# Optimization experiments

Hardware: AMD Instinct MI355X
Metric: run time of the kernel (lower is better)

Reference implementation:

```python
import jax, jax.numpy as jnp
import numpy as np

N = 100000          # nodes (src == target here)
E = 1600000         # edges, avg degree 16
C_IN = 128
C_OUT = 128
R = 7               # num_edge_types
T = 4               # num_node_types


def setup_inputs() -> dict:
    key = jax.random.key(0)
    ks = jax.random.split(key, 7)
    x = jax.random.normal(ks[0], (N, C_IN), dtype=jnp.float32)
    edge_index = jax.random.randint(ks[1], (2, E), 0, N, dtype=jnp.int32)
    edge_type = jax.random.randint(ks[2], (E,), 0, R, dtype=jnp.int32)
    target_node_type = jax.random.randint(ks[3], (N,), 0, T, dtype=jnp.int32)
    # Linear weights: rel_lins (no bias), root_lins (with bias); torch Linear: y = x @ W.T + b
    rel_w = jax.random.normal(ks[4], (R, C_OUT, C_IN), dtype=jnp.float32) * (1.0 / np.sqrt(C_IN))
    root_w = jax.random.normal(ks[5], (T, C_OUT, C_IN), dtype=jnp.float32) * (1.0 / np.sqrt(C_IN))
    root_b = jax.random.normal(ks[6], (T, C_OUT), dtype=jnp.float32) * 0.01
    return {"x": x, "edge_index": edge_index, "edge_type": edge_type,
            "target_node_type": target_node_type,
            "rel_w": rel_w, "root_w": root_w, "root_b": root_b}


def reference(x, edge_index, edge_type, target_node_type, rel_w, root_w, root_b):
    # Per-edge-type gather -> (bias-free) linear -> scatter-mean.
    # linear commutes with mean (no bias), so aggregate first, then apply W_r.
    n = x.shape[0]
    src, dst = edge_index[0], edge_index[1]
    x_j = x[src]                                   # [E, C_in] gather
    seg = dst.astype(jnp.int32) * R + edge_type    # fused (node, edge_type) segment id
    sums = jax.ops.segment_sum(x_j, seg, num_segments=n * R).reshape(n, R, C_IN)
    cnt = jax.ops.segment_sum(jnp.ones((x_j.shape[0],), x.dtype), seg,
                              num_segments=n * R).reshape(n, R)
    means = sums / jnp.maximum(cnt, 1.0)[:, :, None]   # zero rows stay zero (PyG mean of empty = 0)
    out = jnp.einsum('nrc,roc->no', means, rel_w)       # sum_r rel_lins[r](mean_r)
    # Per-node-type root linear with bias (small loop over T=4 types).
    for t in range(T):
        m = (target_node_type == t).astype(x.dtype)[:, None]
        out = out + m * (x @ root_w[t].T + root_b[t])
    return out
```

## Files before the change

kernel.cpp:

```cpp
#include <hip/hip_runtime.h>

#define N_NODES 100000
#define N_EDGES 1600000
#define C_DIM   128
#define R_TYPES 7
#define T_TYPES 4
#define SEGS    (N_NODES * R_TYPES)
#define NB_E    (N_EDGES / 256)
#define NB_N    ((N_NODES + 255) / 256)
#define XP_ROWS 100096
#define DST_PART 12500
#define NB_ROOT ((N_NODES + 63) / 64)

#define OFF_CNTI   0ull
#define OFF_INV    2800000ull
#define OFF_DOFF   5600000ull
#define OFF_CURS   6000004ull
#define OFF_MISC   6400004ull
#define OFF_PERM   6400132ull
#define PERM_CAP   100288
#define OFF_BLKN   6801284ull
#define OFF_BSUM   6813796ull
#define OFF_ESRC   6815360ull
#define OFF_XP     13215360ull
#define OFF_WF     38839936ull
#define OFF_XWB    39069312ull
#define XWB_PLANE  ((size_t)XP_ROWS * 128)
#define FULL_NEED  218441344ull
#define FB_NEED    64693888ull
#define OFF_WRF    OFF_PERM

typedef __attribute__((ext_vector_type(8))) short short8;
typedef __attribute__((ext_vector_type(4))) float f32x4;

__device__ inline unsigned short f2bf(float f) {
    unsigned int u = __float_as_uint(f);
    u += 0x7fffu + ((u >> 16) & 1u);
    return (unsigned short)(u >> 16);
}
__device__ inline float bf2f(unsigned int h) { return __uint_as_float(h << 16); }

__global__ void edge_hist(const int* __restrict__ ei, const int* __restrict__ et,
                          int* __restrict__ cnti) {
    int e = blockIdx.x * 256 + threadIdx.x;
    atomicAdd(&cnti[ei[N_EDGES + e] * R_TYPES + et[e]], 1);
}

__global__ void inv_kernel(const int* __restrict__ cnti, float* __restrict__ inv) {
    int i = blockIdx.x * blockDim.x + threadIdx.x;
    if (i < SEGS) inv[i] = 1.0f / (float)max(cnti[i], 1);
}

__global__ void dst_scan1(const int* __restrict__ cnti, int* __restrict__ dst_off,
                          int* __restrict__ bsum) {
    __shared__ int sbuf[256];
    int tid = threadIdx.x;
    int i = blockIdx.x * 256 + tid;
    int v = 0;
    if (i < N_NODES) {
        #pragma unroll
        for (int r = 0; r < R_TYPES; ++r) v += cnti[i * R_TYPES + r];
    }
    sbuf[tid] = v;
    __syncthreads();
    #pragma unroll
    for (int off = 1; off < 256; off <<= 1) {
        int t = (tid >= off) ? sbuf[tid - off] : 0;
        __syncthreads();
        sbuf[tid] += t;
        __syncthreads();
    }
    int incl = sbuf[tid];
    if (i < N_NODES) dst_off[i] = incl - v;
    if (tid == 255) bsum[blockIdx.x] = incl;
}

__global__ void seg_scan2(int* __restrict__ bsum, int nb) {
    __shared__ int sbuf[256];
    int tid = threadIdx.x;
    int running = 0;
    for (int c0 = 0; c0 < nb; c0 += 256) {
        int b = c0 + tid;
        int v = (b < nb) ? bsum[b] : 0;
        sbuf[tid] = v;
        __syncthreads();
        #pragma unroll
        for (int off = 1; off < 256; off <<= 1) {
            int t = (tid >= off) ? sbuf[tid - off] : 0;
            __syncthreads();
            sbuf[tid] += t;
            __syncthreads();
        }
        int incl = sbuf[tid];
        int tot = sbuf[255];
        __syncthreads();
        if (b < nb) bsum[b] = running + incl - v;
        running += tot;
    }
}

__global__ void dst_scan3(int* __restrict__ dst_off, int* __restrict__ cursor,
                          const int* __restrict__ bsum) {
    int i = blockIdx.x * 256 + threadIdx.x;
    if (i < N_NODES) {
        int val = dst_off[i] + bsum[blockIdx.x];
        dst_off[i] = val;
        cursor[i] = val;
    }
    if (i == 0) dst_off[N_NODES] = N_EDGES;
}

__global__ void place_edges(const int* __restrict__ ei, const int* __restrict__ et,
                            int* __restrict__ cursor, int* __restrict__ esrc) {
    int p = blockIdx.x & 7;
    int e = (blockIdx.x >> 3) * 256 + threadIdx.x;
    int d = ei[N_EDGES + e];
    if (d / DST_PART != p) return;
    int pos = atomicAdd(&cursor[d], 1);
    int r = et[e];
    esrc[pos] = (r << 20) | (r * XP_ROWS + ei[e]);
}

__global__ void cvt_x_frag(const float* __restrict__ x, unsigned short* __restrict__ xp) {
    int id = blockIdx.x * 256 + threadIdx.x;
    int n = id >> 4, ko = id & 15;
    short8 o;
    if (n < N_NODES) {
        const float4* px = (const float4*)(x + (size_t)n * C_DIM + ko * 8);
        float4 a = px[0], b = px[1];
        o[0] = (short)f2bf(a.x); o[1] = (short)f2bf(a.y);
        o[2] = (short)f2bf(a.z); o[3] = (short)f2bf(a.w);
        o[4] = (short)f2bf(b.x); o[5] = (short)f2bf(b.y);
        o[6] = (short)f2bf(b.z); o[7] = (short)f2bf(b.w);
    } else {
        o = (short8)0;
    }
    size_t off = (size_t)(n >> 4) * 2048 + (ko >> 2) * 512 + (ko & 3) * 128 + (n & 15) * 8;
    *(short8*)(xp + off) = o;
}

__global__ void cvt_w_frag(const float* __restrict__ rel_w, unsigned short* __restrict__ wf) {
    int id = blockIdx.x * 256 + threadIdx.x;
    if (id >= R_TYPES * 128 * 16) return;
    int r = id >> 11, rest = id & 2047;
    int o = rest >> 4, ko = rest & 15;
    const float4* pw = (const float4*)(rel_w + (size_t)r * 16384 + o * 128 + ko * 8);
    float4 a = pw[0], b = pw[1];
    short8 v;
    v[0] = (short)f2bf(a.x); v[1] = (short)f2bf(a.y);
    v[2] = (short)f2bf(a.z); v[3] = (short)f2bf(a.w);
    v[4] = (short)f2bf(b.x); v[5] = (short)f2bf(b.y);
    v[6] = (short)f2bf(b.z); v[7] = (short)f2bf(b.w);
    size_t off = (size_t)r * 16384 + (o >> 4) * 2048 + (ko >> 2) * 512 + (ko & 3) * 128 + (o & 15) * 8;
    *(short8*)(wf + off) = v;
}

__global__ void cvt_rootw_frag(const float* __restrict__ root_w, unsigned short* __restrict__ wrf) {
    int id = blockIdx.x * 256 + threadIdx.x;
    if (id >= T_TYPES * 128 * 16) return;
    int t = id >> 11, rest = id & 2047;
    int o = rest >> 4, ko = rest & 15;
    const float4* pw = (const float4*)(root_w + (size_t)t * 16384 + o * 128 + ko * 8);
    float4 a = pw[0], b = pw[1];
    float v[8] = {a.x, a.y, a.z, a.w, b.x, b.y, b.z, b.w};
    short8 hi, lo;
    #pragma unroll
    for (int j = 0; j < 8; ++j) {
        unsigned short h = f2bf(v[j]);
        hi[j] = (short)h;
        lo[j] = (short)f2bf(v[j] - bf2f(h));
    }
    size_t off = (size_t)t * 16384 + (o >> 4) * 2048 + (ko >> 2) * 512 + (ko & 3) * 128 + (o & 15) * 8;
    *(short8*)(wrf + off) = hi;
    *(short8*)(wrf + (size_t)T_TYPES * 16384 + off) = lo;
}

__launch_bounds__(256)
__global__ void root_nat(const float* __restrict__ x, const unsigned short* __restrict__ wrf,
                         const float* __restrict__ root_b, const int* __restrict__ tnt,
                         float* __restrict__ out) {
    __shared__ int cnt[T_TYPES];
    __shared__ int goff[T_TYPES];
    __shared__ int rankb[64];
    __shared__ int lidx[112];
    __shared__ int ttyp[8];
    __shared__ int ntile_s;
    int tid = threadIdx.x;
    int base = blockIdx.x * 64;
    if (tid < T_TYPES) cnt[tid] = 0;
    if (tid < 112) lidx[tid] = -1;
    __syncthreads();
    int myt = -1;
    if (tid < 64 && base + tid < N_NODES) {
        myt = tnt[base + tid];
        rankb[tid] = atomicAdd(&cnt[myt], 1);
    }
    __syncthreads();
    if (tid == 0) {
        int s = 0;
        for (int t = 0; t < T_TYPES; ++t) {
            goff[t] = s;
            int nt = (cnt[t] + 15) >> 4;
            for (int k = 0; k < nt; ++k) ttyp[(s >> 4) + k] = t;
            s += nt << 4;
        }
        ntile_s = s >> 4;
    }
    __syncthreads();
    if (myt >= 0) lidx[goff[myt] + rankb[tid]] = base + tid;
    __syncthreads();
    int ntiles = ntile_s;

    int wave = tid >> 6, lane = tid & 63;
    int l16 = lane & 15, kq = lane >> 4;
    for (int tile = wave; tile < ntiles; tile += 4) {
        int t = ttyp[tile];
        int node = lidx[tile * 16 + l16];
        short8 ah[4], al[4];
        #pragma unroll
        for (int kb = 0; kb < 4; ++kb) {
            float v[8];
            if (node >= 0) {
                const float4* px = (const float4*)(x + (size_t)node * C_DIM + kb * 32 + kq * 8);
                float4 p0 = px[0], p1 = px[1];
                v[0] = p0.x; v[1] = p0.y; v[2] = p0.z; v[3] = p0.w;
                v[4] = p1.x; v[5] = p1.y; v[6] = p1.z; v[7] = p1.w;
            } else {
                #pragma unroll
                for (int j = 0; j < 8; ++j) v[j] = 0.0f;
            }
            #pragma unroll
            for (int j = 0; j < 8; ++j) {
                unsigned short h = f2bf(v[j]);
                ah[kb][j] = (short)h;
                al[kb][j] = (short)f2bf(v[j] - bf2f(h));
            }
        }
        const unsigned short* wh = wrf + (size_t)t * 16384;
        const unsigned short* wl = wh + (size_t)T_TYPES * 16384;
        #pragma unroll
        for (int ct = 0; ct < 8; ++ct) {
            f32x4 acc = (f32x4)0.0f;
            #pragma unroll
            for (int kb = 0; kb < 4; ++kb) {
                short8 bh = *(const short8*)(wh + ct * 2048 + kb * 512 + lane * 8);
                short8 bl = *(const short8*)(wl + ct * 2048 + kb * 512 + lane * 8);
                acc = __builtin_amdgcn_mfma_f32_16x16x32_bf16(ah[kb], bh, acc, 0, 0, 0);
                acc = __builtin_amdgcn_mfma_f32_16x16x32_bf16(al[kb], bh, acc, 0, 0, 0);
                acc = __builtin_amdgcn_mfma_f32_16x16x32_bf16(ah[kb], bl, acc, 0, 0, 0);
            }
            float bias = root_b[t * 128 + ct * 16 + l16];
            #pragma unroll
            for (int i = 0; i < 4; ++i) {
                int nr = lidx[tile * 16 + kq * 4 + i];
                if (nr >= 0)
                    out[(size_t)nr * C_DIM + ct * 16 + l16] = acc[i] + bias;
            }
        }
    }
}

__launch_bounds__(256)
__global__ void xw_gemm_all(const unsigned short* __restrict__ xp,
                            const unsigned short* __restrict__ wf,
                            unsigned short* __restrict__ xwb7) {
    int wave = threadIdx.x >> 6, lane = threadIdx.x & 63;
    int m0 = blockIdx.x * 128;

    short8 a[4][2];
    #pragma unroll
    for (int kb = 0; kb < 4; ++kb)
        #pragma unroll
        for (int rt = 0; rt < 2; ++rt) {
            size_t rtile = (size_t)blockIdx.x * 8 + wave * 2 + rt;
            a[kb][rt] = *(const short8*)(xp + rtile * 2048 + kb * 512 + lane * 8);
        }

    int col = lane & 15, rq = (lane >> 4) * 4;
    for (int r = 0; r < R_TYPES; ++r) {
        const unsigned short* wr = wf + (size_t)r * 16384;
        unsigned short* xwb = xwb7 + (size_t)r * XWB_PLANE;
        #pragma unroll
        for (int ct = 0; ct < 8; ++ct) {
            f32x4 acc0 = (f32x4)0.0f, acc1 = (f32x4)0.0f;
            #pragma unroll
            for (int kb = 0; kb < 4; ++kb) {
                short8 b = *(const short8*)(wr + (size_t)ct * 2048 + kb * 512 + lane * 8);
                acc0 = __builtin_amdgcn_mfma_f32_16x16x32_bf16(a[kb][0], b, acc0, 0, 0, 0);
                acc1 = __builtin_amdgcn_mfma_f32_16x16x32_bf16(a[kb][1], b, acc1, 0, 0, 0);
            }
            #pragma unroll
            for (int i = 0; i < 4; ++i) {
                int n0 = m0 + wave * 32 + rq + i;
                if (n0 < N_NODES)
                    xwb[(size_t)n0 * C_DIM + ct * 16 + col] = f2bf(acc0[i]);
                int n1 = n0 + 16;
                if (n1 < N_NODES)
                    xwb[(size_t)n1 * C_DIM + ct * 16 + col] = f2bf(acc1[i]);
            }
        }
    }
}

__launch_bounds__(256)
__global__ void xw_gemm_mfma(const unsigned short* __restrict__ xp,
                             const unsigned short* __restrict__ wf,
                             unsigned short* __restrict__ xwb, int r) {
    int wave = threadIdx.x >> 6, lane = threadIdx.x & 63;
    int m0 = blockIdx.x * 128;
    const unsigned short* wr = wf + (size_t)r * 16384;

    short8 a[4][2];
    #pragma unroll
    for (int kb = 0; kb < 4; ++kb)
        #pragma unroll
        for (int rt = 0; rt < 2; ++rt) {
            size_t rtile = (size_t)blockIdx.x * 8 + wave * 2 + rt;
            a[kb][rt] = *(const short8*)(xp + rtile * 2048 + kb * 512 + lane * 8);
        }

    int col = lane & 15, rq = (lane >> 4) * 4;
    #pragma unroll
    for (int ct = 0; ct < 8; ++ct) {
        f32x4 acc0 = (f32x4)0.0f, acc1 = (f32x4)0.0f;
        #pragma unroll
        for (int kb = 0; kb < 4; ++kb) {
            short8 b = *(const short8*)(wr + (size_t)ct * 2048 + kb * 512 + lane * 8);
            acc0 = __builtin_amdgcn_mfma_f32_16x16x32_bf16(a[kb][0], b, acc0, 0, 0, 0);
            acc1 = __builtin_amdgcn_mfma_f32_16x16x32_bf16(a[kb][1], b, acc1, 0, 0, 0);
        }
        #pragma unroll
        for (int i = 0; i < 4; ++i) {
            int n0 = m0 + wave * 32 + rq + i;
            if (n0 < N_NODES)
                xwb[(size_t)n0 * C_DIM + ct * 16 + col] = f2bf(acc0[i]);
            int n1 = n0 + 16;
            if (n1 < N_NODES)
                xwb[(size_t)n1 * C_DIM + ct * 16 + col] = f2bf(acc1[i]);
        }
    }
}

__global__ void gather_fused(const int* __restrict__ dst_off, const int* __restrict__ esrc,
                             const float* __restrict__ inv,
                             const unsigned short* __restrict__ xwb7,
                             float* __restrict__ out) {
    int wave = threadIdx.x >> 6, lane = threadIdx.x & 63;
    int d = blockIdx.x * 4 + wave;
    if (d >= N_NODES) return;
    int o0 = dst_off[d], o1 = dst_off[d + 1];
    int q = lane >> 4;
    int l16 = lane & 15;
    const float* invd = inv + d * R_TYPES;

    float4 prev = make_float4(0.f, 0.f, 0.f, 0.f);
    int fidx = (l16 << 1) | q;
    if (lane < 32) prev = ((const float4*)(out + (size_t)d * C_DIM))[fidx];

    float acc[8];
    #pragma unroll
    for (int j = 0; j < 8; ++j) acc[j] = 0.f;

    int e = o0;
    int pkA = 0, pkB = 0;
    bool run = (e + 8 <= o1);
    if (run) { pkA = esrc[e + q]; pkB = esrc[e + 4 + q]; }
    while (run) {
        uint4 rA = *(const uint4*)(xwb7 + (size_t)(pkA & 0xFFFFF) * C_DIM + l16 * 8);
        uint4 rB = *(const uint4*)(xwb7 + (size_t)(pkB & 0xFFFFF) * C_DIM + l16 * 8);
        float sA = invd[pkA >> 20];
        float sB = invd[pkB >> 20];
        e += 8;
        run = (e + 8 <= o1);
        if (run) { pkA = esrc[e + q]; pkB = esrc[e + 4 + q]; }
        acc[0] += bf2f(rA.x & 0xffffu) * sA;  acc[1] += bf2f(rA.x >> 16) * sA;
        acc[2] += bf2f(rA.y & 0xffffu) * sA;  acc[3] += bf2f(rA.y >> 16) * sA;
        acc[4] += bf2f(rA.z & 0xffffu) * sA;  acc[5] += bf2f(rA.z >> 16) * sA;
        acc[6] += bf2f(rA.w & 0xffffu) * sA;  acc[7] += bf2f(rA.w >> 16) * sA;
        acc[0] += bf2f(rB.x & 0xffffu) * sB;  acc[1] += bf2f(rB.x >> 16) * sB;
        acc[2] += bf2f(rB.y & 0xffffu) * sB;  acc[3] += bf2f(rB.y >> 16) * sB;
        acc[4] += bf2f(rB.z & 0xffffu) * sB;  acc[5] += bf2f(rB.z >> 16) * sB;
        acc[6] += bf2f(rB.w & 0xffffu) * sB;  acc[7] += bf2f(rB.w >> 16) * sB;
    }
    for (; e < o1; e += 4) {
        int idx = e + q;
        bool valid = idx < o1;
        int pk = esrc[valid ? idx : e];
        uint4 rw = *(const uint4*)(xwb7 + (size_t)(pk & 0xFFFFF) * C_DIM + l16 * 8);
        float s = valid ? invd[pk >> 20] : 0.0f;
        acc[0] += bf2f(rw.x & 0xffffu) * s;  acc[1] += bf2f(rw.x >> 16) * s;
        acc[2] += bf2f(rw.y & 0xffffu) * s;  acc[3] += bf2f(rw.y >> 16) * s;
        acc[4] += bf2f(rw.z & 0xffffu) * s;  acc[5] += bf2f(rw.z >> 16) * s;
        acc[6] += bf2f(rw.w & 0xffffu) * s;  acc[7] += bf2f(rw.w >> 16) * s;
    }

    #pragma unroll
    for (int j = 0; j < 8; ++j) {
        acc[j] += __shfl_xor(acc[j], 16);
        acc[j] += __shfl_xor(acc[j], 32);
    }
    if (lane < 32) {
        float4 w;
        if (lane < 16)
            w = make_float4(acc[0] + prev.x, acc[1] + prev.y, acc[2] + prev.z, acc[3] + prev.w);
        else
            w = make_float4(acc[4] + prev.x, acc[5] + prev.y, acc[6] + prev.z, acc[7] + prev.w);
        ((float4*)(out + (size_t)d * C_DIM))[fidx] = w;
    }
}

__global__ void gather_rel_f(const int* __restrict__ dst_off, const int* __restrict__ esrc,
                             const float* __restrict__ inv,
                             const unsigned short* __restrict__ xwb,
                             float* __restrict__ out, int rf) {
    int wave = threadIdx.x >> 6, lane = threadIdx.x & 63;
    int d = blockIdx.x * 4 + wave;
    if (d >= N_NODES) return;
    int o0 = dst_off[d], o1 = dst_off[d + 1];
    float ax = 0.0f, ay = 0.0f;
    bool any = false;
    for (int e = o0; e < o1; ++e) {
        int pk = esrc[e];
        if ((pk >> 20) != rf) continue;
        any = true;
        int src = (pk & 0xFFFFF) - rf * XP_ROWS;
        unsigned int row = *(const unsigned int*)(xwb + (size_t)src * C_DIM + lane * 2);
        ax += bf2f(row & 0xffffu);
        ay += bf2f(row >> 16);
    }
    if (!any) return;
    float sc = inv[d * R_TYPES + rf];
    float2* po = (float2*)(out + (size_t)d * C_DIM) + lane;
    float2 v = *po;
    v.x += ax * sc;
    v.y += ay * sc;
    *po = v;
}

extern "C" void kernel_launch(void* const* d_in, const int* in_sizes, int n_in,
                              void* d_out, int out_size, void* d_ws, size_t ws_size,
                              hipStream_t stream) {
    const float* x      = (const float*)d_in[0];
    const int*   ei     = (const int*)d_in[1];
    const int*   et     = (const int*)d_in[2];
    const int*   tnt    = (const int*)d_in[3];
    const float* rel_w  = (const float*)d_in[4];
    const float* root_w = (const float*)d_in[5];
    const float* root_b = (const float*)d_in[6];
    float* out = (float*)d_out;

    char* ws = (char*)d_ws;
    int*   cnti    = (int*)(ws + OFF_CNTI);
    float* inv     = (float*)(ws + OFF_INV);
    int*   dst_off = (int*)(ws + OFF_DOFF);
    int*   cursor  = (int*)(ws + OFF_CURS);
    int*   bsum    = (int*)(ws + OFF_BSUM);
    int*   esrc    = (int*)(ws + OFF_ESRC);
    unsigned short* xp  = (unsigned short*)(ws + OFF_XP);
    unsigned short* wf  = (unsigned short*)(ws + OFF_WF);
    unsigned short* xwb = (unsigned short*)(ws + OFF_XWB);
    unsigned short* wrf = (unsigned short*)(ws + OFF_WRF);

    const bool full = (ws_size >= FULL_NEED);

    hipMemsetAsync(ws + OFF_CNTI, 0, SEGS * sizeof(int), stream);

    cvt_rootw_frag<<<32, 256, 0, stream>>>(root_w, wrf);
    root_nat<<<NB_ROOT, 256, 0, stream>>>(x, wrf, root_b, tnt, out);

    edge_hist  <<<NB_E, 256, 0, stream>>>(ei, et, cnti);
    inv_kernel <<<(SEGS + 255) / 256, 256, 0, stream>>>(cnti, inv);
    dst_scan1  <<<NB_N, 256, 0, stream>>>(cnti, dst_off, bsum);
    seg_scan2  <<<1, 256, 0, stream>>>(bsum, NB_N);
    dst_scan3  <<<NB_N, 256, 0, stream>>>(dst_off, cursor, bsum);
    place_edges<<<NB_E * 8, 256, 0, stream>>>(ei, et, cursor, esrc);

    cvt_x_frag<<<(XP_ROWS * 16) / 256, 256, 0, stream>>>(x, xp);
    cvt_w_frag<<<56, 256, 0, stream>>>(rel_w, wf);

    if (full) {
        xw_gemm_all <<<XP_ROWS / 128, 256, 0, stream>>>(xp, wf, xwb);
        gather_fused<<<(N_NODES + 3) / 4, 256, 0, stream>>>(dst_off, esrc, inv, xwb, out);
    } else {
        for (int r = 0; r < R_TYPES; ++r) {
            xw_gemm_mfma<<<XP_ROWS / 128, 256, 0, stream>>>(xp, wf, xwb, r);
            gather_rel_f<<<(N_NODES + 3) / 4, 256, 0, stream>>>(dst_off, esrc, inv, xwb, out, r);
        }
    }
}
```

Measured before the change: 470.3 us.

## Fuse x bf16 conversion into GEMM, reorder root linear, unroll gather deeper

```diff
diff --git a/kernel.cpp b/kernel.cpp
--- a/kernel.cpp
+++ b/kernel.cpp
@@ -119,24 +119,6 @@
     int pos = atomicAdd(&cursor[d], 1);
     int r = et[e];
     esrc[pos] = (r << 20) | (r * XP_ROWS + ei[e]);
-}
-
-__global__ void cvt_x_frag(const float* __restrict__ x, unsigned short* __restrict__ xp) {
-    int id = blockIdx.x * 256 + threadIdx.x;
-    int n = id >> 4, ko = id & 15;
-    short8 o;
-    if (n < N_NODES) {
-        const float4* px = (const float4*)(x + (size_t)n * C_DIM + ko * 8);
-        float4 a = px[0], b = px[1];
-        o[0] = (short)f2bf(a.x); o[1] = (short)f2bf(a.y);
-        o[2] = (short)f2bf(a.z); o[3] = (short)f2bf(a.w);
-        o[4] = (short)f2bf(b.x); o[5] = (short)f2bf(b.y);
-        o[6] = (short)f2bf(b.z); o[7] = (short)f2bf(b.w);
-    } else {
-        o = (short8)0;
-    }
-    size_t off = (size_t)(n >> 4) * 2048 + (ko >> 2) * 512 + (ko & 3) * 128 + (n & 15) * 8;
-    *(short8*)(xp + off) = o;
 }
 
 __global__ void cvt_w_frag(const float* __restrict__ rel_w, unsigned short* __restrict__ wf) {
@@ -253,30 +235,46 @@
             #pragma unroll
             for (int i = 0; i < 4; ++i) {
                 int nr = lidx[tile * 16 + kq * 4 + i];
-                if (nr >= 0)
-                    out[(size_t)nr * C_DIM + ct * 16 + l16] = acc[i] + bias;
+                if (nr >= 0) {
+                    float* po = out + (size_t)nr * C_DIM + ct * 16 + l16;
+                    *po += acc[i] + bias;
+                }
             }
         }
     }
 }
 
 __launch_bounds__(256)
-__global__ void xw_gemm_all(const unsigned short* __restrict__ xp,
+__global__ void xw_gemm_all(const float* __restrict__ x,
                             const unsigned short* __restrict__ wf,
                             unsigned short* __restrict__ xwb7) {
     int wave = threadIdx.x >> 6, lane = threadIdx.x & 63;
     int m0 = blockIdx.x * 128;
+    int l16 = lane & 15, kq = lane >> 4;
 
     short8 a[4][2];
     #pragma unroll
-    for (int kb = 0; kb < 4; ++kb)
-        #pragma unroll
-        for (int rt = 0; rt < 2; ++rt) {
-            size_t rtile = (size_t)blockIdx.x * 8 + wave * 2 + rt;
-            a[kb][rt] = *(const short8*)(xp + rtile * 2048 + kb * 512 + lane * 8);
-        }
-
-    int col = lane & 15, rq = (lane >> 4) * 4;
+    for (int rt = 0; rt < 2; ++rt) {
+        int row = m0 + wave * 32 + rt * 16 + l16;
+        bool ok = row < N_NODES;
+        #pragma unroll
+        for (int kb = 0; kb < 4; ++kb) {
+            float v[8];
+            if (ok) {
+                const float4* px = (const float4*)(x + (size_t)row * C_DIM + kb * 32 + kq * 8);
+                float4 p0 = px[0], p1 = px[1];
+                v[0] = p0.x; v[1] = p0.y; v[2] = p0.z; v[3] = p0.w;
+                v[4] = p1.x; v[5] = p1.y; v[6] = p1.z; v[7] = p1.w;
+            } else {
+                #pragma unroll
+                for (int j = 0; j < 8; ++j) v[j] = 0.0f;
+            }
+            #pragma unroll
+            for (int j = 0; j < 8; ++j) a[kb][rt][j] = (short)f2bf(v[j]);
+        }
+    }
+
+    int col = l16, rq = kq * 4;
     for (int r = 0; r < R_TYPES; ++r) {
         const unsigned short* wr = wf + (size_t)r * 16384;
         unsigned short* xwb = xwb7 + (size_t)r * XWB_PLANE;
@@ -303,23 +301,37 @@
 }
 
 __launch_bounds__(256)
-__global__ void xw_gemm_mfma(const unsigned short* __restrict__ xp,
+__global__ void xw_gemm_mfma(const float* __restrict__ x,
                              const unsigned short* __restrict__ wf,
                              unsigned short* __restrict__ xwb, int r) {
     int wave = threadIdx.x >> 6, lane = threadIdx.x & 63;
     int m0 = blockIdx.x * 128;
+    int l16 = lane & 15, kq = lane >> 4;
     const unsigned short* wr = wf + (size_t)r * 16384;
 
     short8 a[4][2];
     #pragma unroll
-    for (int kb = 0; kb < 4; ++kb)
-        #pragma unroll
-        for (int rt = 0; rt < 2; ++rt) {
-            size_t rtile = (size_t)blockIdx.x * 8 + wave * 2 + rt;
-            a[kb][rt] = *(const short8*)(xp + rtile * 2048 + kb * 512 + lane * 8);
-        }
-
-    int col = lane & 15, rq = (lane >> 4) * 4;
+    for (int rt = 0; rt < 2; ++rt) {
+        int row = m0 + wave * 32 + rt * 16 + l16;
+        bool ok = row < N_NODES;
+        #pragma unroll
+        for (int kb = 0; kb < 4; ++kb) {
+            float v[8];
+            if (ok) {
+                const float4* px = (const float4*)(x + (size_t)row * C_DIM + kb * 32 + kq * 8);
+                float4 p0 = px[0], p1 = px[1];
+                v[0] = p0.x; v[1] = p0.y; v[2] = p0.z; v[3] = p0.w;
+                v[4] = p1.x; v[5] = p1.y; v[6] = p1.z; v[7] = p1.w;
+            } else {
+                #pragma unroll
+                for (int j = 0; j < 8; ++j) v[j] = 0.0f;
+            }
+            #pragma unroll
+            for (int j = 0; j < 8; ++j) a[kb][rt][j] = (short)f2bf(v[j]);
+        }
+    }
+
+    int col = l16, rq = kq * 4;
     #pragma unroll
     for (int ct = 0; ct < 8; ++ct) {
         f32x4 acc0 = (f32x4)0.0f, acc1 = (f32x4)0.0f;
@@ -352,46 +364,63 @@
     int q = lane >> 4;
     int l16 = lane & 15;
     const float* invd = inv + d * R_TYPES;
-
-    float4 prev = make_float4(0.f, 0.f, 0.f, 0.f);
-    int fidx = (l16 << 1) | q;
-    if (lane < 32) prev = ((const float4*)(out + (size_t)d * C_DIM))[fidx];
-
     float acc[8];
     #pragma unroll
     for (int j = 0; j < 8; ++j) acc[j] = 0.f;
 
     int e = o0;
-    int pkA = 0, pkB = 0;
-    bool run = (e + 8 <= o1);
-    if (run) { pkA = esrc[e + q]; pkB = esrc[e + 4 + q]; }
+    int pk0 = 0, pk1 = 0, pk2 = 0, pk3 = 0;
+    bool run = (e + 16 <= o1);
+    if (run) {
+        pk0 = esrc[e + q];       pk1 = esrc[e + 4 + q];
+        pk2 = esrc[e + 8 + q];   pk3 = esrc[e + 12 + q];
+    }
     while (run) {
-        uint4 rA = *(const uint4*)(xwb7 + (size_t)(pkA & 0xFFFFF) * C_DIM + l16 * 8);
-        uint4 rB = *(const uint4*)(xwb7 + (size_t)(pkB & 0xFFFFF) * C_DIM + l16 * 8);
-        float sA = invd[pkA >> 20];
-        float sB = invd[pkB >> 20];
-        e += 8;
-        run = (e + 8 <= o1);
-        if (run) { pkA = esrc[e + q]; pkB = esrc[e + 4 + q]; }
-        acc[0] += bf2f(rA.x & 0xffffu) * sA;  acc[1] += bf2f(rA.x >> 16) * sA;
-        acc[2] += bf2f(rA.y & 0xffffu) * sA;  acc[3] += bf2f(rA.y >> 16) * sA;
-        acc[4] += bf2f(rA.z & 0xffffu) * sA;  acc[5] += bf2f(rA.z >> 16) * sA;
-        acc[6] += bf2f(rA.w & 0xffffu) * sA;  acc[7] += bf2f(rA.w >> 16) * sA;
-        acc[0] += bf2f(rB.x & 0xffffu) * sB;  acc[1] += bf2f(rB.x >> 16) * sB;
-        acc[2] += bf2f(rB.y & 0xffffu) * sB;  acc[3] += bf2f(rB.y >> 16) * sB;
-        acc[4] += bf2f(rB.z & 0xffffu) * sB;  acc[5] += bf2f(rB.z >> 16) * sB;
-        acc[6] += bf2f(rB.w & 0xffffu) * sB;  acc[7] += bf2f(rB.w >> 16) * sB;
-    }
-    for (; e < o1; e += 4) {
-        int idx = e + q;
-        bool valid = idx < o1;
-        int pk = esrc[valid ? idx : e];
-        uint4 rw = *(const uint4*)(xwb7 + (size_t)(pk & 0xFFFFF) * C_DIM + l16 * 8);
-        float s = valid ? invd[pk >> 20] : 0.0f;
-        acc[0] += bf2f(rw.x & 0xffffu) * s;  acc[1] += bf2f(rw.x >> 16) * s;
-        acc[2] += bf2f(rw.y & 0xffffu) * s;  acc[3] += bf2f(rw.y >> 16) * s;
-        acc[4] += bf2f(rw.z & 0xffffu) * s;  acc[5] += bf2f(rw.z >> 16) * s;
-        acc[6] += bf2f(rw.w & 0xffffu) * s;  acc[7] += bf2f(rw.w >> 16) * s;
+        uint4 r0 = *(const uint4*)(xwb7 + (size_t)(pk0 & 0xFFFFF) * C_DIM + l16 * 8);
+        uint4 r1 = *(const uint4*)(xwb7 + (size_t)(pk1 & 0xFFFFF) * C_DIM + l16 * 8);
+        uint4 r2 = *(const uint4*)(xwb7 + (size_t)(pk2 & 0xFFFFF) * C_DIM + l16 * 8);
+        uint4 r3 = *(const uint4*)(xwb7 + (size_t)(pk3 & 0xFFFFF) * C_DIM + l16 * 8);
+        float s0 = invd[pk0 >> 20];
+        float s1 = invd[pk1 >> 20];
+        float s2 = invd[pk2 >> 20];
+        float s3 = invd[pk3 >> 20];
+        e += 16;
+        run = (e + 16 <= o1);
+        if (run) {
+            pk0 = esrc[e + q];       pk1 = esrc[e + 4 + q];
+            pk2 = esrc[e + 8 + q];   pk3 = esrc[e + 12 + q];
+        }
+        acc[0] += bf2f(r0.x & 0xffffu) * s0;  acc[1] += bf2f(r0.x >> 16) * s0;
+        acc[2] += bf2f(r0.y & 0xffffu) * s0;  acc[3] += bf2f(r0.y >> 16) * s0;
+        acc[4] += bf2f(r0.z & 0xffffu) * s0;  acc[5] += bf2f(r0.z >> 16) * s0;
+        acc[6] += bf2f(r0.w & 0xffffu) * s0;  acc[7] += bf2f(r0.w >> 16) * s0;
+        acc[0] += bf2f(r1.x & 0xffffu) * s1;  acc[1] += bf2f(r1.x >> 16) * s1;
+        acc[2] += bf2f(r1.y & 0xffffu) * s1;  acc[3] += bf2f(r1.y >> 16) * s1;
+        acc[4] += bf2f(r1.z & 0xffffu) * s1;  acc[5] += bf2f(r1.z >> 16) * s1;
+        acc[6] += bf2f(r1.w & 0xffffu) * s1;  acc[7] += bf2f(r1.w >> 16) * s1;
+        acc[0] += bf2f(r2.x & 0xffffu) * s2;  acc[1] += bf2f(r2.x >> 16) * s2;
+        acc[2] += bf2f(r2.y & 0xffffu) * s2;  acc[3] += bf2f(r2.y >> 16) * s2;
+        acc[4] += bf2f(r2.z & 0xffffu) * s2;  acc[5] += bf2f(r2.z >> 16) * s2;
+        acc[6] += bf2f(r2.w & 0xffffu) * s2;  acc[7] += bf2f(r2.w >> 16) * s2;
+        acc[0] += bf2f(r3.x & 0xffffu) * s3;  acc[1] += bf2f(r3.x >> 16) * s3;
+        acc[2] += bf2f(r3.y & 0xffffu) * s3;  acc[3] += bf2f(r3.y >> 16) * s3;
+        acc[4] += bf2f(r3.z & 0xffffu) * s3;  acc[5] += bf2f(r3.z >> 16) * s3;
+        acc[6] += bf2f(r3.w & 0xffffu) * s3;  acc[7] += bf2f(r3.w >> 16) * s3;
+    }
+    #pragma unroll
+    for (int j = 0; j < 4; ++j) {
+        int eb = e + j * 4;
+        if (eb < o1) {
+            int idx = eb + q;
+            bool valid = idx < o1;
+            int pk = esrc[valid ? idx : eb];
+            uint4 rw = *(const uint4*)(xwb7 + (size_t)(pk & 0xFFFFF) * C_DIM + l16 * 8);
+            float s = valid ? invd[pk >> 20] : 0.0f;
+            acc[0] += bf2f(rw.x & 0xffffu) * s;  acc[1] += bf2f(rw.x >> 16) * s;
+            acc[2] += bf2f(rw.y & 0xffffu) * s;  acc[3] += bf2f(rw.y >> 16) * s;
+            acc[4] += bf2f(rw.z & 0xffffu) * s;  acc[5] += bf2f(rw.z >> 16) * s;
+            acc[6] += bf2f(rw.w & 0xffffu) * s;  acc[7] += bf2f(rw.w >> 16) * s;
+        }
     }
 
     #pragma unroll
@@ -400,11 +429,9 @@
         acc[j] += __shfl_xor(acc[j], 32);
     }
     if (lane < 32) {
-        float4 w;
-        if (lane < 16)
-            w = make_float4(acc[0] + prev.x, acc[1] + prev.y, acc[2] + prev.z, acc[3] + prev.w);
-        else
-            w = make_float4(acc[4] + prev.x, acc[5] + prev.y, acc[6] + prev.z, acc[7] + prev.w);
+        int fidx = (l16 << 1) | q;
+        float4 w = (lane < 16) ? make_float4(acc[0], acc[1], acc[2], acc[3])
+                               : make_float4(acc[4], acc[5], acc[6], acc[7]);
         ((float4*)(out + (size_t)d * C_DIM))[fidx] = w;
     }
 }
@@ -456,7 +483,6 @@
     int*   cursor  = (int*)(ws + OFF_CURS);
     int*   bsum    = (int*)(ws + OFF_BSUM);
     int*   esrc    = (int*)(ws + OFF_ESRC);
-    unsigned short* xp  = (unsigned short*)(ws + OFF_XP);
     unsigned short* wf  = (unsigned short*)(ws + OFF_WF);
     unsigned short* xwb = (unsigned short*)(ws + OFF_XWB);
     unsigned short* wrf = (unsigned short*)(ws + OFF_WRF);
@@ -464,9 +490,10 @@
     const bool full = (ws_size >= FULL_NEED);
 
     hipMemsetAsync(ws + OFF_CNTI, 0, SEGS * sizeof(int), stream);
+    if (!full)
+        hipMemsetAsync(d_out, 0, (size_t)out_size * sizeof(float), stream);
 
     cvt_rootw_frag<<<32, 256, 0, stream>>>(root_w, wrf);
-    root_nat<<<NB_ROOT, 256, 0, stream>>>(x, wrf, root_b, tnt, out);
 
     edge_hist  <<<NB_E, 256, 0, stream>>>(ei, et, cnti);
     inv_kernel <<<(SEGS + 255) / 256, 256, 0, stream>>>(cnti, inv);
@@ -475,16 +502,16 @@
     dst_scan3  <<<NB_N, 256, 0, stream>>>(dst_off, cursor, bsum);
     place_edges<<<NB_E * 8, 256, 0, stream>>>(ei, et, cursor, esrc);
 
-    cvt_x_frag<<<(XP_ROWS * 16) / 256, 256, 0, stream>>>(x, xp);
     cvt_w_frag<<<56, 256, 0, stream>>>(rel_w, wf);
 
     if (full) {
-        xw_gemm_all <<<XP_ROWS / 128, 256, 0, stream>>>(xp, wf, xwb);
+        xw_gemm_all <<<XP_ROWS / 128, 256, 0, stream>>>(x, wf, xwb);
         gather_fused<<<(N_NODES + 3) / 4, 256, 0, stream>>>(dst_off, esrc, inv, xwb, out);
     } else {
         for (int r = 0; r < R_TYPES; ++r) {
-            xw_gemm_mfma<<<XP_ROWS / 128, 256, 0, stream>>>(xp, wf, xwb, r);
+            xw_gemm_mfma<<<XP_ROWS / 128, 256, 0, stream>>>(x, wf, xwb, r);
             gather_rel_f<<<(N_NODES + 3) / 4, 256, 0, stream>>>(dst_off, esrc, inv, xwb, out, r);
         }
     }
-}
+    root_nat<<<NB_ROOT, 256, 0, stream>>>(x, wrf, root_b, tnt, out);
+}
```

New measurement: 481.1 us. 2.3% more time.
